# Optimization experiments

Hardware: AMD Instinct MI355X
Metric: run time of the kernel (lower is better)

The kernel has to match this reference:

```python
import jax, jax.numpy as jnp
import numpy as np

D_MODEL = 1024
B, S = 4, 4096


def setup_inputs() -> dict:
    key = jax.random.key(0)
    k1, k2, k3, k4, k5 = jax.random.split(key, 5)
    lim = 1.0 / np.sqrt(D_MODEL)  # nn.Linear default init range
    x = jax.random.normal(k1, (B, S, D_MODEL), dtype=jnp.float32)
    mask = jnp.ones((B, S), dtype=jnp.float32)
    W_up = jax.random.uniform(k2, (D_MODEL, D_MODEL), jnp.float32, -lim, lim)
    b_up = jax.random.uniform(k3, (D_MODEL,), jnp.float32, -lim, lim)
    W_f = jax.random.uniform(k4, (D_MODEL, D_MODEL), jnp.float32, -lim, lim)
    b_f = jax.random.uniform(k5, (D_MODEL,), jnp.float32, -lim, lim)
    decay_param = jnp.zeros((1,), dtype=jnp.float32)
    return {"x": x, "mask": mask, "W_up": W_up, "b_up": b_up,
            "W_f": W_f, "b_f": b_f, "decay_param": decay_param}


def _decay_scan(u, decay):
    # h_t = decay * h_{t-1} + u_t  along axis=1, via associative scan.
    # Element: (a, b) representing h -> a*h + b; compose: (a1*a2, b1*a2 + b2).
    a = jnp.broadcast_to(decay, u.shape)

    def combine(c1, c2):
        a1, b1 = c1
        a2, b2 = c2
        return a1 * a2, b1 * a2 + b2

    _, h = jax.lax.associative_scan(combine, (a, u), axis=1)
    return h


def reference(x, mask, W_up, b_up, W_f, b_f, decay_param):
    decay = jax.nn.sigmoid(decay_param)[0]
    # u_i = mask_i * linear_update(x_i)
    u = (jnp.einsum('bsd,ed->bse', x, W_up) + b_up) * mask[..., None]
    # h_t = sum_{i<=t} decay^(t-i) * u_i  (exponential-decay recurrence)
    h = _decay_scan(u, decay)
    return jnp.einsum('bsd,ed->bse', h, W_f) + b_f
```

## Files before the change

kernel.cpp:

```cpp
#include <hip/hip_runtime.h>
#include <hip/hip_bf16.h>
#include <cstdint>
#include <cstddef>

#define DMODEL 1024
#define BATCH  4
#define SEQ    4096
#define BSROWS (BATCH*SEQ)
#define CHUNK  32
#define NCHUNK (SEQ/CHUNK)
#define NCH_T  (BATCH*NCHUNK)

typedef __attribute__((ext_vector_type(8))) short bf16x8;
typedef __attribute__((ext_vector_type(4))) float f32x4;


__device__ __forceinline__ unsigned short f2bf(float f) {
  union { float f; uint32_t u; } v; v.f = f;
  uint32_t u = v.u;
  u += 0x7FFFu + ((u >> 16) & 1u);
  return (unsigned short)(u >> 16);
}

__device__ __forceinline__ float sigmoid_dev(const float* dp) {
  return 1.0f / (1.0f + expf(-dp[0]));
}

typedef __attribute__((address_space(1))) void void_g;
typedef __attribute__((address_space(3))) void void_l;

__device__ __forceinline__ void gl2lds16(const void* g, void* l) {
  __builtin_amdgcn_global_load_lds((void_g*)g, (void_l*)l, 16, 0, 0);
}

__device__ __forceinline__ void kloop64(
    const unsigned short* __restrict__ A, const unsigned short* __restrict__ B,
    int m0, int n0, f32x4 acc[2][2],
    unsigned short* As, unsigned short* Bs, int tid) {
  int lane = tid & 63, w = tid >> 6, wm = w & 1, wn = w >> 1;
  int quad = lane >> 4, l16 = lane & 15;
  int r = tid >> 3, cch = tid & 7;
  int g = cch ^ (r & 7);

  auto stage = [&](int t, int slot) {
    int k0 = t * 64;
    unsigned short* dA = As + slot * 4096;
    unsigned short* dB = Bs + slot * 4096;
    gl2lds16(A + (size_t)(m0 + r) * DMODEL + k0 + g * 8,      dA + r * 64 + cch * 8);
    gl2lds16(A + (size_t)(m0 + 32 + r) * DMODEL + k0 + g * 8, dA + (32 + r) * 64 + cch * 8);
    gl2lds16(B + (size_t)(n0 + r) * DMODEL + k0 + g * 8,      dB + r * 64 + cch * 8);
    gl2lds16(B + (size_t)(n0 + 32 + r) * DMODEL + k0 + g * 8, dB + (32 + r) * 64 + cch * 8);
  };
  auto compute = [&](int slot) {
    const bf16x8* Av = (const bf16x8*)(As + slot * 4096);
    const bf16x8* Bv = (const bf16x8*)(Bs + slot * 4096);
    #pragma unroll
    for (int kk = 0; kk < 2; ++kk) {
      bf16x8 af[2], bfr[2];
      #pragma unroll
      for (int i = 0; i < 2; ++i) {
        int rowA = wm * 32 + i * 16 + l16;
        af[i]  = Av[rowA * 8 + ((kk * 4 + quad) ^ (l16 & 7))];
        int rowB = wn * 32 + i * 16 + l16;
        bfr[i] = Bv[rowB * 8 + ((kk * 4 + quad) ^ (l16 & 7))];
      }
      __builtin_amdgcn_s_setprio(1);
      #pragma unroll
      for (int i = 0; i < 2; ++i)
        #pragma unroll
        for (int j = 0; j < 2; ++j)
          acc[i][j] = __builtin_amdgcn_mfma_f32_16x16x32_bf16(af[i], bfr[j], acc[i][j], 0, 0, 0);
      __builtin_amdgcn_s_setprio(0);
    }
  };

  stage(0, 0); stage(1, 1);
  asm volatile("s_waitcnt vmcnt(4)" ::: "memory");
  __builtin_amdgcn_s_barrier();
  asm volatile("" ::: "memory");
  int cur = 0;
  for (int t = 0; t < 14; ++t) {
    int ns = cur + 2; if (ns >= 3) ns -= 3;
    stage(t + 2, ns);
    compute(cur);
    asm volatile("s_waitcnt vmcnt(4)" ::: "memory");
    __builtin_amdgcn_s_barrier();
    asm volatile("" ::: "memory");
    cur = (cur == 2) ? 0 : cur + 1;
  }
  compute(cur);
  asm volatile("s_waitcnt vmcnt(0)" ::: "memory");
  __builtin_amdgcn_s_barrier();
  asm volatile("" ::: "memory");
  cur = (cur == 2) ? 0 : cur + 1;
  compute(cur);
}

__global__ __launch_bounds__(256) void prep_kernel(
    const float* __restrict__ x, const float* __restrict__ mask,
    const float* __restrict__ W_up, const float* __restrict__ b_up,
    const float* __restrict__ W_f, const float* __restrict__ dp,
    unsigned short* __restrict__ Wf_bf, unsigned short* __restrict__ WupT,
    float* __restrict__ bb, unsigned short* __restrict__ hv,
    float* __restrict__ carry, float* __restrict__ lbeta,
    float* __restrict__ cbeta) {
  __shared__ float tile[32][33];
  int blk = blockIdx.x;
  int tid = threadIdx.x;

  if (blk < 512) {
    float decay = sigmoid_dev(dp);
    int b = blk / NCHUNK, c = blk % NCHUNK;
    int base = b * SEQ + c * CHUNK;
    const float4* xp = (const float4*)(x + (size_t)base * DMODEL);
    const float4* mp4 = (const float4*)(mask + base);
    float mreg[32];
    #pragma unroll
    for (int q = 0; q < 8; ++q) {
      float4 t = mp4[q];
      mreg[q * 4 + 0] = t.x; mreg[q * 4 + 1] = t.y;
      mreg[q * 4 + 2] = t.z; mreg[q * 4 + 3] = t.w;
    }
    float4 h = make_float4(0.f, 0.f, 0.f, 0.f);
    #pragma unroll
    for (int s = 0; s < CHUNK; ++s) {
      float m = mreg[s];
      float4 xv = xp[(size_t)s * (DMODEL / 4) + tid];
      h.x = decay * h.x + m * xv.x;
      h.y = decay * h.y + m * xv.y;
      h.z = decay * h.z + m * xv.z;
      h.w = decay * h.w + m * xv.w;
      ushort4 o;
      o.x = f2bf(h.x); o.y = f2bf(h.y); o.z = f2bf(h.z); o.w = f2bf(h.w);
      ((ushort4*)hv)[(size_t)(base + s) * (DMODEL / 4) + tid] = o;
    }
    ((float4*)carry)[(size_t)blk * (DMODEL / 4) + tid] = h;
  } else if (blk < 1536) {
    int e = blk - 512;
    int lane = tid & 63, w = tid >> 6;
    float4 v = ((const float4*)(W_f + (size_t)e * DMODEL))[tid];
    float4 bu = ((const float4*)b_up)[tid];
    ushort4 o;
    o.x = f2bf(v.x); o.y = f2bf(v.y); o.z = f2bf(v.z); o.w = f2bf(v.w);
    ((ushort4*)(Wf_bf + (size_t)e * DMODEL))[tid] = o;
    float s = v.x * bu.x + v.y * bu.y + v.z * bu.z + v.w * bu.w;
    #pragma unroll
    for (int off = 32; off; off >>= 1) s += __shfl_down(s, off);
    if (lane == 0) ((float*)tile)[w] = s;
    __syncthreads();
    if (tid == 0)
      bb[e] = ((float*)tile)[0] + ((float*)tile)[1] +
              ((float*)tile)[2] + ((float*)tile)[3];
  } else if (blk < 2560) {
    int id = blk - 1536;
    int bx = id & 31, by = id >> 5;
    int tx = tid & 31, ty = tid >> 5;
    int xx = bx * 32 + tx;
    int y0 = by * 32;
    for (int j = ty; j < 32; j += 8)
      tile[j][tx] = W_up[(size_t)(y0 + j) * DMODEL + xx];
    __syncthreads();
    int ox = by * 32 + tx;
    int oy0 = bx * 32;
    for (int j = ty; j < 32; j += 8)
      WupT[(size_t)(oy0 + j) * DMODEL + ox] = f2bf(tile[tx][j]);
  } else {
    float decay = sigmoid_dev(dp);
    int t = (blk - 2560) * 256 + tid;
    int s = t & 31;
    int cbase = t & ~31;
    float hb = 0.f;
    for (int i = 0; i <= s; ++i)
      hb = decay * hb + mask[cbase + i];
    lbeta[t] = hb;
    if (s == 31) cbeta[t >> 5] = hb;
  }
}

__global__ __launch_bounds__(256) void mid2_kernel(
    const unsigned short* __restrict__ Wf_bf,
    const unsigned short* __restrict__ WupT,
    unsigned short* __restrict__ Wc,
    const float* __restrict__ carry, const float* __restrict__ cbeta,
    const float* __restrict__ dp,
    unsigned short* __restrict__ Pbf, float* __restrict__ pbeta) {
  __shared__ unsigned short As[3 * 64 * 64];
  __shared__ unsigned short Bs[3 * 64 * 64];
  int tid = threadIdx.x;
  if (blockIdx.x < 256) {
    int mt = blockIdx.x >> 4, nt = blockIdx.x & 15;
    f32x4 acc[2][2] = {};
    kloop64(Wf_bf, WupT, mt * 64, nt * 64, acc, As, Bs, tid);
    int lane = tid & 63, w = tid >> 6, wm = w & 1, wn = w >> 1;
    int quad = lane >> 4, l16 = lane & 15;
    #pragma unroll
    for (int j = 0; j < 2; ++j) {
      int col = nt * 64 + wn * 32 + j * 16 + l16;
      #pragma unroll
      for (int i = 0; i < 2; ++i) {
        int rowb = mt * 64 + wm * 32 + i * 16 + quad * 4;
        #pragma unroll
        for (int rr = 0; rr < 4; ++rr)
          Wc[(size_t)(rowb + rr) * DMODEL + col] = f2bf(acc[i][j][rr]);
      }
    }
  } else {
    float decay = sigmoid_dev(dp);
    float dL = powf(decay, (float)CHUNK);
    int gid = (blockIdx.x - 256) * 256 + tid;
    int b = gid >> 10, dd = gid & 1023;
    float P = 0.f;
    for (int c0 = 0; c0 < NCHUNK; c0 += 8) {
      float v[8];
      #pragma unroll
      for (int j = 0; j < 8; ++j)
        v[j] = carry[(size_t)(b * NCHUNK + c0 + j) * DMODEL + dd];
      #pragma unroll
      for (int j = 0; j < 8; ++j) {
        Pbf[(size_t)(b * NCHUNK + c0 + j) * DMODEL + dd] = f2bf(P);
        P = dL * P + v[j];
      }
    }
    if (dd == 0) {
      float Pb = 0.f;
      for (int c0 = 0; c0 < NCHUNK; c0 += 16) {
        float v[16];
        #pragma unroll
        for (int j = 0; j < 16; ++j) v[j] = cbeta[b * NCHUNK + c0 + j];
        #pragma unroll
        for (int j = 0; j < 16; ++j) {
          pbeta[b * NCHUNK + c0 + j] = Pb;
          Pb = dL * Pb + v[j];
        }
      }
    }
  }
}

__global__ __launch_bounds__(256) void pout_kernel(
    const unsigned short* __restrict__ Pbf,
    const unsigned short* __restrict__ Wc,
    const float* __restrict__ pbeta, const float* __restrict__ bb,
    float* __restrict__ Pout) {
  __shared__ unsigned short As[3 * 64 * 64];
  __shared__ unsigned short Bs[3 * 64 * 64];
  int tid = threadIdx.x;
  int mt = blockIdx.x >> 4, nt = blockIdx.x & 15;
  f32x4 acc[2][2] = {};
  kloop64(Pbf, Wc, mt * 64, nt * 64, acc, As, Bs, tid);
  int lane = tid & 63, w = tid >> 6, wm = w & 1, wn = w >> 1;
  int quad = lane >> 4, l16 = lane & 15;
  #pragma unroll
  for (int j = 0; j < 2; ++j) {
    int col = nt * 64 + wn * 32 + j * 16 + l16;
    float bbv = bb[col];
    #pragma unroll
    for (int i = 0; i < 2; ++i) {
      int rowb = mt * 64 + wm * 32 + i * 16 + quad * 4;
      #pragma unroll
      for (int rr = 0; rr < 4; ++rr) {
        int row = rowb + rr;
        Pout[(size_t)row * DMODEL + col] = acc[i][j][rr] + pbeta[row] * bbv;
      }
    }
  }
}

__global__ __launch_bounds__(512) void gemm_main(
    const unsigned short* __restrict__ A,
    const unsigned short* __restrict__ Bm,
    const float* __restrict__ Pout,
    const float* __restrict__ lbeta,
    const float* __restrict__ bb,
    const float* __restrict__ bias_f,
    const float* __restrict__ dp,
    float* __restrict__ out) {
  __shared__ unsigned short As[4 * 256 * 32];
  __shared__ unsigned short Bs[4 * 256 * 32];
  __shared__ float dpow[CHUNK];
  const int SLOT = 256 * 32;
  int tid = threadIdx.x;
  if (tid < CHUNK) {
    float decay = sigmoid_dev(dp);
    dpow[tid] = powf(decay, (float)(tid + 1));
  }
  __syncthreads();

  int lane = tid & 63, wid = tid >> 6;
  int wm = wid >> 2, wn = wid & 3;
  int quad = lane >> 4, l16 = lane & 15;
  int phi = (l16 >> 1) & 3;
  int r = tid >> 2, c4 = tid & 3;
  int g = c4 ^ ((r >> 1) & 3);

  int bid = blockIdx.x;
  int xcd = bid & 7, jb = bid >> 3;
  int m0 = (xcd * 8 + (jb >> 2)) * 256;
  int n0 = (jb & 3) * 256;

  f32x4 acc[8][4] = {};

  auto stageA = [&](int t, int slot) {
    int k0 = t * 32;
    unsigned short* dA = As + slot * SLOT;
    gl2lds16(A + (size_t)(m0 + r) * DMODEL + k0 + g * 8,        dA + r * 32 + c4 * 8);
    gl2lds16(A + (size_t)(m0 + 128 + r) * DMODEL + k0 + g * 8,  dA + (128 + r) * 32 + c4 * 8);
  };
  auto stageB = [&](int t, int slot) {
    int k0 = t * 32;
    unsigned short* dB = Bs + slot * SLOT;
    gl2lds16(Bm + (size_t)(n0 + r) * DMODEL + k0 + g * 8,       dB + r * 32 + c4 * 8);
    gl2lds16(Bm + (size_t)(n0 + 128 + r) * DMODEL + k0 + g * 8, dB + (128 + r) * 32 + c4 * 8);
  };

  bf16x8 bfr[4];
  auto phase = [&](int slot, int mh, bool loadB) {
    const bf16x8* Av = (const bf16x8*)(As + slot * SLOT);
    const bf16x8* Bv = (const bf16x8*)(Bs + slot * SLOT);
    bf16x8 af[4];
    #pragma unroll
    for (int i = 0; i < 4; ++i) {
      int rowA = wm * 128 + mh * 64 + i * 16 + l16;
      af[i] = Av[rowA * 4 + (quad ^ phi)];
    }
    if (loadB) {
      #pragma unroll
      for (int j = 0; j < 4; ++j) {
        int rowB = wn * 64 + j * 16 + l16;
        bfr[j] = Bv[rowB * 4 + (quad ^ phi)];
      }
    }
    __builtin_amdgcn_s_setprio(1);
    #pragma unroll
    for (int i = 0; i < 4; ++i)
      #pragma unroll
      for (int j = 0; j < 4; ++j)
        acc[mh * 4 + i][j] =
            __builtin_amdgcn_mfma_f32_16x16x32_bf16(af[i], bfr[j], acc[mh * 4 + i][j], 0, 0, 0);
    __builtin_amdgcn_s_setprio(0);
  };

  stageA(0, 0); stageB(0, 0);
  stageA(1, 1); stageB(1, 1);
  stageA(2, 2); stageB(2, 2);
  asm volatile("s_waitcnt vmcnt(8)" ::: "memory");
  __builtin_amdgcn_s_barrier();
  asm volatile("" ::: "memory");

  for (int t = 0; t < 29; ++t) {
    int cs = t & 3;
    int ss = (t + 3) & 3;
    stageA(t + 3, ss);
    phase(cs, 0, true);
    stageB(t + 3, ss);
    phase(cs, 1, false);
    asm volatile("s_waitcnt vmcnt(8)" ::: "memory");
    __builtin_amdgcn_s_barrier();
    asm volatile("" ::: "memory");
  }
  phase(1, 0, true);  phase(1, 1, false);
  asm volatile("s_waitcnt vmcnt(4)" ::: "memory");
  __builtin_amdgcn_s_barrier();
  asm volatile("" ::: "memory");
  phase(2, 0, true);  phase(2, 1, false);
  asm volatile("s_waitcnt vmcnt(0)" ::: "memory");
  __builtin_amdgcn_s_barrier();
  asm volatile("" ::: "memory");
  phase(3, 0, true);  phase(3, 1, false);

  float bbv[4], bfv[4];
  #pragma unroll
  for (int j = 0; j < 4; ++j) {
    int col = n0 + wn * 64 + j * 16 + l16;
    bbv[j] = bb[col];
    bfv[j] = bias_f[col];
  }
  #pragma unroll
  for (int i = 0; i < 8; ++i) {
    #pragma unroll
    for (int rr = 0; rr < 4; ++rr) {
      int row = m0 + wm * 128 + i * 16 + quad * 4 + rr;
      float lb  = lbeta[row];
      float dpw = dpow[row & 31];
      const float* poRow = Pout + (size_t)(row >> 5) * DMODEL;
      float* outRow = out + (size_t)row * DMODEL;
      #pragma unroll
      for (int j = 0; j < 4; ++j) {
        int col = n0 + wn * 64 + j * 16 + l16;
        outRow[col] = acc[i][j][rr] + dpw * poRow[col] + lb * bbv[j] + bfv[j];
      }
    }
  }
}


extern "C" void kernel_launch(void* const* d_in, const int* in_sizes, int n_in,
                              void* d_out, int out_size, void* d_ws, size_t ws_size,
                              hipStream_t stream) {
  const float* x    = (const float*)d_in[0];
  const float* mask = (const float*)d_in[1];
  const float* W_up = (const float*)d_in[2];
  const float* b_up = (const float*)d_in[3];
  const float* W_f  = (const float*)d_in[4];
  const float* b_f  = (const float*)d_in[5];
  const float* dp   = (const float*)d_in[6];
  float* out = (float*)d_out;

  char* ws = (char*)d_ws;
  unsigned short* hv    = (unsigned short*)(ws);
  unsigned short* Wc    = (unsigned short*)(ws + 33554432);
  unsigned short* Wf_bf = (unsigned short*)(ws + 35651584);
  unsigned short* WupT  = (unsigned short*)(ws + 37748736);
  float* carry  = (float*)(ws + 39845888);
  unsigned short* Pbf = (unsigned short*)(ws + 41943040);
  float* Pout   = (float*)(ws + 42991616);
  float* lbeta  = (float*)(ws + 45088768);
  float* cbeta  = (float*)(ws + 45154304);
  float* pbeta  = (float*)(ws + 45156352);
  float* bb     = (float*)(ws + 45158400);

  prep_kernel<<<2624, 256, 0, stream>>>(x, mask, W_up, b_up, W_f, dp,
                                        Wf_bf, WupT, bb, hv, carry, lbeta, cbeta);
  mid2_kernel<<<272, 256, 0, stream>>>(Wf_bf, WupT, Wc, carry, cbeta, dp,
                                       Pbf, pbeta);
  pout_kernel<<<128, 256, 0, stream>>>(Pbf, Wc, pbeta, bb, Pout);
  gemm_main<<<256, 512, 0, stream>>>(hv, Wc, Pout, lbeta, bb, b_f, dp, out);
}
```

Measured before the change: 189.6 us.

## Restructure GEMM main loop into ping-pong phases and parallelize prep kernels

```diff
diff --git a/kernel.cpp b/kernel.cpp
--- a/kernel.cpp
+++ b/kernel.cpp
@@ -160,20 +160,28 @@
     for (int j = ty; j < 32; j += 8)
       tile[j][tx] = W_up[(size_t)(y0 + j) * DMODEL + xx];
     __syncthreads();
-    int ox = by * 32 + tx;
-    int oy0 = bx * 32;
-    for (int j = ty; j < 32; j += 8)
-      WupT[(size_t)(oy0 + j) * DMODEL + ox] = f2bf(tile[tx][j]);
+    int dd = tid >> 3;
+    int c4 = (tid & 7) * 4;
+    ushort4 o;
+    o.x = f2bf(tile[c4 + 0][dd]);
+    o.y = f2bf(tile[c4 + 1][dd]);
+    o.z = f2bf(tile[c4 + 2][dd]);
+    o.w = f2bf(tile[c4 + 3][dd]);
+    *(ushort4*)(WupT + (size_t)(bx * 32 + dd) * DMODEL + y0 + c4) = o;
   } else {
     float decay = sigmoid_dev(dp);
     int t = (blk - 2560) * 256 + tid;
     int s = t & 31;
-    int cbase = t & ~31;
-    float hb = 0.f;
-    for (int i = 0; i <= s; ++i)
-      hb = decay * hb + mask[cbase + i];
-    lbeta[t] = hb;
-    if (s == 31) cbeta[t >> 5] = hb;
+    float h = mask[t];
+    float wgt = decay;
+    #pragma unroll
+    for (int off = 1; off < 32; off <<= 1) {
+      float up = __shfl_up(h, off);
+      if (s >= off) h += wgt * up;
+      wgt = wgt * wgt;
+    }
+    lbeta[t] = h;
+    if (s == 31) cbeta[t >> 5] = h;
   }
 }
 
@@ -299,6 +307,7 @@
   int n0 = (jb & 3) * 256;
 
   f32x4 acc[8][4] = {};
+  bf16x8 bfr[4];
 
   auto stageA = [&](int t, int slot) {
     int k0 = t * 32;
@@ -312,24 +321,21 @@
     gl2lds16(Bm + (size_t)(n0 + r) * DMODEL + k0 + g * 8,       dB + r * 32 + c4 * 8);
     gl2lds16(Bm + (size_t)(n0 + 128 + r) * DMODEL + k0 + g * 8, dB + (128 + r) * 32 + c4 * 8);
   };
-
-  bf16x8 bfr[4];
-  auto phase = [&](int slot, int mh, bool loadB) {
-    const bf16x8* Av = (const bf16x8*)(As + slot * SLOT);
-    const bf16x8* Bv = (const bf16x8*)(Bs + slot * SLOT);
-    bf16x8 af[4];
+  auto readA = [&](const bf16x8* Av, int mh, bf16x8 af[4]) {
     #pragma unroll
     for (int i = 0; i < 4; ++i) {
       int rowA = wm * 128 + mh * 64 + i * 16 + l16;
       af[i] = Av[rowA * 4 + (quad ^ phi)];
     }
-    if (loadB) {
-      #pragma unroll
-      for (int j = 0; j < 4; ++j) {
-        int rowB = wn * 64 + j * 16 + l16;
-        bfr[j] = Bv[rowB * 4 + (quad ^ phi)];
-      }
-    }
+  };
+  auto readB = [&](const bf16x8* Bv) {
+    #pragma unroll
+    for (int j = 0; j < 4; ++j) {
+      int rowB = wn * 64 + j * 16 + l16;
+      bfr[j] = Bv[rowB * 4 + (quad ^ phi)];
+    }
+  };
+  auto mfma16 = [&](int mh, const bf16x8 af[4]) {
     __builtin_amdgcn_s_setprio(1);
     #pragma unroll
     for (int i = 0; i < 4; ++i)
@@ -348,25 +354,48 @@
   asm volatile("" ::: "memory");
 
   for (int t = 0; t < 29; ++t) {
-    int cs = t & 3;
-    int ss = (t + 3) & 3;
+    int cs = t & 3, ss = (t + 3) & 3;
+    const bf16x8* Av = (const bf16x8*)(As + cs * SLOT);
+    const bf16x8* Bv = (const bf16x8*)(Bs + cs * SLOT);
+    bf16x8 af[4];
+    readA(Av, 0, af);
+    readB(Bv);
     stageA(t + 3, ss);
-    phase(cs, 0, true);
+    __builtin_amdgcn_s_barrier();
+    asm volatile("s_waitcnt lgkmcnt(0)" ::: "memory");
+    __builtin_amdgcn_sched_barrier(0);
+    mfma16(0, af);
+    __builtin_amdgcn_s_barrier();
+    bf16x8 af2[4];
+    readA(Av, 1, af2);
     stageB(t + 3, ss);
-    phase(cs, 1, false);
     asm volatile("s_waitcnt vmcnt(8)" ::: "memory");
     __builtin_amdgcn_s_barrier();
+    asm volatile("s_waitcnt lgkmcnt(0)" ::: "memory");
+    __builtin_amdgcn_sched_barrier(0);
+    mfma16(1, af2);
+    __builtin_amdgcn_s_barrier();
     asm volatile("" ::: "memory");
   }
-  phase(1, 0, true);  phase(1, 1, false);
+  auto tailfull = [&](int slot) {
+    const bf16x8* Av = (const bf16x8*)(As + slot * SLOT);
+    const bf16x8* Bv = (const bf16x8*)(Bs + slot * SLOT);
+    bf16x8 af[4];
+    readA(Av, 0, af);
+    readB(Bv);
+    mfma16(0, af);
+    readA(Av, 1, af);
+    mfma16(1, af);
+  };
+  tailfull(1);
   asm volatile("s_waitcnt vmcnt(4)" ::: "memory");
   __builtin_amdgcn_s_barrier();
   asm volatile("" ::: "memory");
-  phase(2, 0, true);  phase(2, 1, false);
+  tailfull(2);
   asm volatile("s_waitcnt vmcnt(0)" ::: "memory");
   __builtin_amdgcn_s_barrier();
   asm volatile("" ::: "memory");
-  phase(3, 0, true);  phase(3, 1, false);
+  tailfull(3);
 
   float bbv[4], bfv[4];
   #pragma unroll
```

After: 193.9 us. +2.2%, slower.
